# Kernel optimization log

Measured on AMD Instinct MI355X. Metric: run time of the kernel, lower is better.

## Reference

```python
import jax, jax.numpy as jnp
import numpy as np

B, N, D_IN, D_OUT = 4, 2048, 4096, 4096
E, R, D_ATT = 8, 16, 128
SCALING = 16.0 / 16.0  # alpha / rank


def setup_inputs() -> dict:
    key = jax.random.key(0)
    ks = jax.random.split(key, 8)
    x = jax.random.normal(ks[0], (B, N, D_IN), dtype=jnp.float32)
    weight = jax.random.normal(ks[1], (D_OUT, D_IN), dtype=jnp.float32) * 0.02  # frozen base
    bias = jax.random.normal(ks[2], (D_OUT,), dtype=jnp.float32) * 0.02
    router_V = jax.random.normal(ks[3], (D_ATT, D_IN), dtype=jnp.float32) * 0.02
    router_U = jax.random.normal(ks[4], (D_ATT, D_IN), dtype=jnp.float32) * 0.02
    router_W = jax.random.normal(ks[5], (E, D_ATT), dtype=jnp.float32) * 0.02
    experts_A = jax.random.normal(ks[6], (E, D_IN, R), dtype=jnp.float32) * 0.01
    experts_B = jax.random.normal(ks[7], (E, R, D_OUT), dtype=jnp.float32) * 0.01
    return {"x": x, "weight": weight, "bias": bias, "router_V": router_V,
            "router_U": router_U, "router_W": router_W,
            "experts_A": experts_A, "experts_B": experts_B}


def reference(x, weight, bias, router_V, router_U, router_W, experts_A, experts_B):
    # Frozen base projection: F.linear(x, weight, bias)
    base = jnp.einsum('bnd,od->bno', x, weight) + bias
    # ABMIL gated-attention router
    v = jnp.tanh(jnp.einsum('bnd,ad->bna', x, router_V))            # [B,N,D_att]
    u = jax.nn.sigmoid(jnp.einsum('bnd,ad->bna', x, router_U))      # [B,N,D_att]
    scores = jnp.einsum('bna,ea->bne', v * u, router_W)             # [B,N,E]
    router_weights = jax.nn.sigmoid(scores)                         # independent sigmoid gates
    # Per-expert low-rank path (dropout is identity at inference / p=0)
    lora_down = jnp.einsum('bnd,edr->bner', x, experts_A)           # [B,N,E,R]
    weighted = lora_down * router_weights[..., None]
    moe_out = jnp.einsum('bner,erd->bnd', weighted, experts_B)      # [B,N,D_out]
    return base + SCALING * moe_out
```

## Files before the change

### kernel.cpp

```cpp
#include <hip/hip_runtime.h>
#include <hip/hip_bf16.h>

#define M_TOT   8192
#define D_IN    4096
#define D_OUT   4096
#define N_E     8
#define N_R     16
#define D_ATT   128
#define ER      128
#define CATN    384
#define KEXT    4224

typedef __attribute__((ext_vector_type(8))) __bf16 bf16x8;
typedef __attribute__((ext_vector_type(4))) float  f32x4;

__device__ __forceinline__ ushort f2bf(float f) {
  union { float f; unsigned u; } v; v.f = f;
  unsigned r = (v.u + 0x7fffu + ((v.u >> 16) & 1u)) >> 16;
  return (ushort)r;
}

__global__ void f2bf4_kernel(const float* __restrict__ in, ushort* __restrict__ out, long n4) {
  long i = blockIdx.x * (long)blockDim.x + threadIdx.x;
  if (i >= n4) return;
  const float4 a = reinterpret_cast<const float4*>(in)[i];
  ushort4 r; r.x = f2bf(a.x); r.y = f2bf(a.y); r.z = f2bf(a.z); r.w = f2bf(a.w);
  reinterpret_cast<ushort4*>(out)[i] = r;
}

__global__ void f2bf4s_kernel(const float* __restrict__ in, ushort* __restrict__ out, long n4) {
  long i = blockIdx.x * (long)blockDim.x + threadIdx.x;
  if (i >= n4) return;
  const float4 a = reinterpret_cast<const float4*>(in)[i];
  ushort4 r; r.x = f2bf(a.x); r.y = f2bf(a.y); r.z = f2bf(a.z); r.w = f2bf(a.w);
  long row = i >> 10, c4 = (i & 1023) << 2;
  *reinterpret_cast<ushort4*>(out + row * KEXT + c4) = r;
}

__global__ void prep_catA_kernel(const float* __restrict__ expA, ushort* __restrict__ cat) {
  int idx = blockIdx.x * 256 + threadIdx.x;
  int j = idx >> 12, d = idx & 4095;
  int e = j >> 4, r = j & 15;
  cat[(size_t)(2 * D_ATT + j) * D_IN + d] = f2bf(expA[((size_t)e * D_IN + d) * N_R + r]);
}

__global__ void prep_bt_kernel(const float* __restrict__ expB, ushort* __restrict__ we) {
  int idx = blockIdx.x * 256 + threadIdx.x;
  int j = idx >> 12, o = idx & 4095;
  we[(size_t)o * KEXT + D_IN + j] = f2bf(expB[(size_t)j * D_OUT + o]);
}

__global__ void gate_kernel(const float* __restrict__ P, const float* __restrict__ rW,
                            ushort* __restrict__ wtd) {
  int token = blockIdx.x * 4 + (threadIdx.x >> 6);
  int l = threadIdx.x & 63;
  const float* p = P + (size_t)token * CATN;
  float v0 = tanhf(p[l]);
  float v1 = tanhf(p[l + 64]);
  float u0 = 1.f / (1.f + __expf(-p[D_ATT + l]));
  float u1 = 1.f / (1.f + __expf(-p[D_ATT + l + 64]));
  float g0 = v0 * u0, g1 = v1 * u1;
  float rw[8];
  #pragma unroll
  for (int e = 0; e < 8; ++e) {
    float s = g0 * rW[e * D_ATT + l] + g1 * rW[e * D_ATT + l + 64];
    #pragma unroll
    for (int off = 32; off > 0; off >>= 1) s += __shfl_xor(s, off);
    rw[e] = 1.f / (1.f + __expf(-s));
  }
  int q = l >> 4;
  float rw_a = (q == 0) ? rw[0] : (q == 1) ? rw[1] : (q == 2) ? rw[2] : rw[3];
  float rw_b = (q == 0) ? rw[4] : (q == 1) ? rw[5] : (q == 2) ? rw[6] : rw[7];
  wtd[(size_t)token * KEXT + l]      = f2bf(p[2 * D_ATT + l]      * rw_a);
  wtd[(size_t)token * KEXT + l + 64] = f2bf(p[2 * D_ATT + l + 64] * rw_b);
}

__global__ __launch_bounds__(256, 2)
void gemm128_kernel(const ushort* __restrict__ A, const ushort* __restrict__ Bm,
                    float* __restrict__ C, int Ncols, int K, int lda, int ldb)
{
  __shared__ ushort As[128 * 64];
  __shared__ ushort Bs[128 * 64];
  const int tid = threadIdx.x;
  const int w = tid >> 6, l = tid & 63;
  const int wr = w >> 1, wc = w & 1;
  const int l16 = l & 15, lq = l >> 4;
  const int brow = blockIdx.y * 128;
  const int bcol = blockIdx.x * 128;

  f32x4 acc[4][4] = {};
  const int nk = K >> 6;

  for (int kt = 0; kt < nk; ++kt) {
    int k0 = kt << 6;
    #pragma unroll
    for (int c = 0; c < 4; ++c) {
      int rloc = w * 32 + c * 8;
      int rl = rloc + (l >> 3);
      int kk = k0 + (l & 7) * 8;
      const ushort* ga = A  + (size_t)(brow + rl) * lda + kk;
      const ushort* gb = Bm + (size_t)(bcol + rl) * ldb + kk;
      __builtin_amdgcn_global_load_lds((const __attribute__((address_space(1))) void*)ga,
                                       (__attribute__((address_space(3))) void*)(As + rloc * 64),
                                       16, 0, 0);
      __builtin_amdgcn_global_load_lds((const __attribute__((address_space(1))) void*)gb,
                                       (__attribute__((address_space(3))) void*)(Bs + rloc * 64),
                                       16, 0, 0);
    }
    __syncthreads();

    #pragma unroll
    for (int ks = 0; ks < 2; ++ks) {
      bf16x8 af[4], bfv[4];
      #pragma unroll
      for (int mi = 0; mi < 4; ++mi)
        af[mi] = *reinterpret_cast<const bf16x8*>(As + (wr * 64 + mi * 16 + l16) * 64 + ks * 32 + lq * 8);
      #pragma unroll
      for (int ni = 0; ni < 4; ++ni)
        bfv[ni] = *reinterpret_cast<const bf16x8*>(Bs + (wc * 64 + ni * 16 + l16) * 64 + ks * 32 + lq * 8);
      #pragma unroll
      for (int mi = 0; mi < 4; ++mi)
        #pragma unroll
        for (int ni = 0; ni < 4; ++ni)
          acc[mi][ni] = __builtin_amdgcn_mfma_f32_16x16x32_bf16(af[mi], bfv[ni], acc[mi][ni], 0, 0, 0);
    }
    __syncthreads();
  }

  #pragma unroll
  for (int ni = 0; ni < 4; ++ni) {
    int col = bcol + wc * 64 + ni * 16 + l16;
    #pragma unroll
    for (int mi = 0; mi < 4; ++mi) {
      f32x4 v = acc[mi][ni];
      int row0 = brow + wr * 64 + mi * 16 + lq * 4;
      #pragma unroll
      for (int j = 0; j < 4; ++j)
        C[(size_t)(row0 + j) * Ncols + col] = v[j];
    }
  }
}

__global__ __launch_bounds__(512, 2)
void gemm256_kernel(const ushort* __restrict__ A, const ushort* __restrict__ Bm,
                    float* __restrict__ C, const float* __restrict__ bias,
                    int Ncols, int K, int ld, int ntm)
{
  __shared__ ushort lds[2][2][2][8192];
  const int tid = threadIdx.x;
  const int wid = tid >> 6, l = tid & 63;
  const int wr = wid >> 2, wc = wid & 3;
  const int l16 = l & 15, lq = l >> 4;
  const int rxor = (l16 & 7) << 3;

  const int cpx = gridDim.x >> 3;
  const int sid = ((int)blockIdx.x & 7) * cpx + ((int)blockIdx.x >> 3);
  const int brow = (sid % ntm) * 256;
  const int bcol = (sid / ntm) * 256;

  const int NT = K >> 6;

  const int srow = tid >> 3;
  const int scol = (((tid & 7) ^ ((tid >> 3) & 7)) << 3);

#define STAGE(buf_, mat_, half_, kt_) do {                                        \
    const ushort* _s = (mat_) ? Bm : A;                                           \
    int _rb = ((mat_) ? bcol : brow) + (half_) * 128 + srow;                      \
    ushort* _d = &lds[(buf_)][(mat_)][(half_)][wid * 512];                        \
    _Pragma("unroll")                                                             \
    for (int _c = 0; _c < 2; ++_c) {                                              \
      const ushort* _g = _s + (size_t)(_rb + _c * 64) * ld + (kt_) * 64 + scol;   \
      __builtin_amdgcn_global_load_lds(                                           \
          (const __attribute__((address_space(1))) void*)_g,                      \
          (__attribute__((address_space(3))) void*)(_d + _c * 4096), 16, 0, 0);   \
    } } while (0)

#define LDA_FRAG(buf_, mi_, ks_) \
  (*reinterpret_cast<const bf16x8*>(&lds[(buf_)][0][wr][((mi_) * 16 + l16) * 64 + (((ks_) * 32 + lq * 8) ^ rxor)]))
#define LDB_FRAG(buf_, ni_, ks_) \
  (*reinterpret_cast<const bf16x8*>(&lds[(buf_)][1][wc >> 1][((wc & 1) * 64 + (ni_) * 16 + l16) * 64 + (((ks_) * 32 + lq * 8) ^ rxor)]))

  f32x4 acc[8][4] = {};

  STAGE(0, 0, 0, 0); STAGE(0, 0, 1, 0);
  STAGE(0, 1, 0, 0); STAGE(0, 1, 1, 0);
  {
    const int k1 = (NT > 1) ? 1 : 0;
    STAGE(1, 1, 0, k1); STAGE(1, 1, 1, k1);
  }
  asm volatile("s_waitcnt vmcnt(4)" ::: "memory");
  __builtin_amdgcn_s_barrier();

  for (int t = 0; t < NT; ++t) {
    const int buf = t & 1;
    const int ktA = (t + 1 < NT) ? t + 1 : NT - 1;
    const int ktB = (t + 2 < NT) ? t + 2 : NT - 1;
    bf16x8 af[4][2], b0[2][2], b1[2][2];

    #pragma unroll
    for (int mi = 0; mi < 4; ++mi)
      #pragma unroll
      for (int ks = 0; ks < 2; ++ks)
        af[mi][ks] = LDA_FRAG(buf, mi, ks);
    #pragma unroll
    for (int ni = 0; ni < 2; ++ni)
      #pragma unroll
      for (int ks = 0; ks < 2; ++ks)
        b0[ni][ks] = LDB_FRAG(buf, ni, ks);
    STAGE(buf ^ 1, 0, 0, ktA);
    __builtin_amdgcn_s_barrier();
    asm volatile("s_waitcnt lgkmcnt(0)" ::: "memory");
    __builtin_amdgcn_s_setprio(1);
    #pragma unroll
    for (int mi = 0; mi < 4; ++mi)
      #pragma unroll
      for (int ni = 0; ni < 2; ++ni)
        #pragma unroll
        for (int ks = 0; ks < 2; ++ks)
          acc[mi][ni] = __builtin_amdgcn_mfma_f32_16x16x32_bf16(af[mi][ks], b0[ni][ks], acc[mi][ni], 0, 0, 0);
    __builtin_amdgcn_s_setprio(0);
    __builtin_amdgcn_s_barrier();

    #pragma unroll
    for (int ni = 0; ni < 2; ++ni)
      #pragma unroll
      for (int ks = 0; ks < 2; ++ks)
        b1[ni][ks] = LDB_FRAG(buf, ni + 2, ks);
    STAGE(buf ^ 1, 0, 1, ktA);
    __builtin_amdgcn_s_barrier();
    asm volatile("s_waitcnt lgkmcnt(0)" ::: "memory");
    __builtin_amdgcn_s_setprio(1);
    #pragma unroll
    for (int mi = 0; mi < 4; ++mi)
      #pragma unroll
      for (int ni = 0; ni < 2; ++ni)
        #pragma unroll
        for (int ks = 0; ks < 2; ++ks)
          acc[mi][ni + 2] = __builtin_amdgcn_mfma_f32_16x16x32_bf16(af[mi][ks], b1[ni][ks], acc[mi][ni + 2], 0, 0, 0);
    __builtin_amdgcn_s_setprio(0);
    __builtin_amdgcn_s_barrier();

    #pragma unroll
    for (int mi = 0; mi < 4; ++mi)
      #pragma unroll
      for (int ks = 0; ks < 2; ++ks)
        af[mi][ks] = LDA_FRAG(buf, mi + 4, ks);
    STAGE(buf, 1, 0, ktB);
    __builtin_amdgcn_s_barrier();
    asm volatile("s_waitcnt lgkmcnt(0)" ::: "memory");
    __builtin_amdgcn_s_setprio(1);
    #pragma unroll
    for (int mi = 0; mi < 4; ++mi)
      #pragma unroll
      for (int ni = 0; ni < 2; ++ni)
        #pragma unroll
        for (int ks = 0; ks < 2; ++ks)
          acc[mi + 4][ni + 2] = __builtin_amdgcn_mfma_f32_16x16x32_bf16(af[mi][ks], b1[ni][ks], acc[mi + 4][ni + 2], 0, 0, 0);
    __builtin_amdgcn_s_setprio(0);
    __builtin_amdgcn_s_barrier();

    STAGE(buf, 1, 1, ktB);
    asm volatile("s_waitcnt vmcnt(4)" ::: "memory");
    __builtin_amdgcn_s_barrier();
    __builtin_amdgcn_s_setprio(1);
    #pragma unroll
    for (int mi = 0; mi < 4; ++mi)
      #pragma unroll
      for (int ni = 0; ni < 2; ++ni)
        #pragma unroll
        for (int ks = 0; ks < 2; ++ks)
          acc[mi + 4][ni] = __builtin_amdgcn_mfma_f32_16x16x32_bf16(af[mi][ks], b0[ni][ks], acc[mi + 4][ni], 0, 0, 0);
    __builtin_amdgcn_s_setprio(0);
    __builtin_amdgcn_s_barrier();
  }

  asm volatile("s_waitcnt vmcnt(0)" ::: "memory");

  #pragma unroll
  for (int ni = 0; ni < 4; ++ni) {
    int col = bcol + wc * 64 + ni * 16 + l16;
    float bs = bias[col];
    #pragma unroll
    for (int mi = 0; mi < 8; ++mi) {
      int row0 = brow + wr * 128 + mi * 16 + lq * 4;
      #pragma unroll
      for (int j = 0; j < 4; ++j)
        C[(size_t)(row0 + j) * Ncols + col] = acc[mi][ni][j] + bs;
    }
  }
#undef STAGE
#undef LDA_FRAG
#undef LDB_FRAG
}

extern "C" void kernel_launch(void* const* d_in, const int* in_sizes, int n_in,
                              void* d_out, int out_size, void* d_ws, size_t ws_size,
                              hipStream_t stream) {
  const float* x      = (const float*)d_in[0];
  const float* weight = (const float*)d_in[1];
  const float* bias   = (const float*)d_in[2];
  const float* rV     = (const float*)d_in[3];
  const float* rU     = (const float*)d_in[4];
  const float* rW     = (const float*)d_in[5];
  const float* expA   = (const float*)d_in[6];
  const float* expB   = (const float*)d_in[7];
  float* out = (float*)d_out;

  ushort* xe  = (ushort*)d_ws;
  ushort* we  = xe  + (size_t)M_TOT * KEXT;
  ushort* cat = we  + (size_t)D_OUT * KEXT;
  float*  P   = (float*)(cat + (size_t)CATN * D_IN);

  long n4;
  n4 = (long)M_TOT * D_IN / 4;
  f2bf4s_kernel<<<dim3((n4 + 255) / 256), 256, 0, stream>>>(x, xe, n4);
  n4 = (long)D_OUT * D_IN / 4;
  f2bf4s_kernel<<<dim3((n4 + 255) / 256), 256, 0, stream>>>(weight, we, n4);
  n4 = (long)D_ATT * D_IN / 4;
  f2bf4_kernel<<<dim3((n4 + 255) / 256), 256, 0, stream>>>(rV, cat, n4);
  f2bf4_kernel<<<dim3((n4 + 255) / 256), 256, 0, stream>>>(rU, cat + (size_t)D_ATT * D_IN, n4);
  prep_catA_kernel<<<dim3(ER * D_IN / 256), 256, 0, stream>>>(expA, cat);
  prep_bt_kernel<<<dim3(ER * D_OUT / 256), 256, 0, stream>>>(expB, we);

  gemm128_kernel<<<dim3(CATN / 128, M_TOT / 128), 256, 0, stream>>>(
      xe, cat, P, CATN, D_IN, KEXT, D_IN);

  gate_kernel<<<dim3(M_TOT / 4), 256, 0, stream>>>(P, rW, xe + D_IN);

  gemm256_kernel<<<dim3((D_OUT / 256) * (M_TOT / 256)), 512, 0, stream>>>(
      xe, we, out, bias, D_OUT, KEXT, KEXT, M_TOT / 256);
}
```

Measured before the change: 405.1 us.

## Software-pipeline LDS fragment reads across tiles and hardcode GEMM dimensions

Restructures the main 256x256 GEMM loop so the next tile's low A/B fragments are read from LDS during the current tile's last MFMA phase, with ping-pong register sets and a loop unrolled by two. The high-B and high-A fragments are now loaded inside the MFMA phases instead of before the barriers. All shapes and strides become compile-time constants in both GEMMs, which lets the compiler simplify address arithmetic. The intent is to hide LDS read latency behind MFMA work, at the cost of more live fragment registers at two waves per SIMD and a loop that assumes an even tile count.

```diff
diff --git a/kernel.cpp b/kernel.cpp
--- a/kernel.cpp
+++ b/kernel.cpp
@@ -10,6 +10,8 @@
 #define ER      128
 #define CATN    384
 #define KEXT    4224
+#define NTK     66
+#define NTM     32
 
 typedef __attribute__((ext_vector_type(8))) __bf16 bf16x8;
 typedef __attribute__((ext_vector_type(4))) float  f32x4;
@@ -77,7 +79,7 @@
 
 __global__ __launch_bounds__(256, 2)
 void gemm128_kernel(const ushort* __restrict__ A, const ushort* __restrict__ Bm,
-                    float* __restrict__ C, int Ncols, int K, int lda, int ldb)
+                    float* __restrict__ C)
 {
   __shared__ ushort As[128 * 64];
   __shared__ ushort Bs[128 * 64];
@@ -89,17 +91,16 @@
   const int bcol = blockIdx.x * 128;
 
   f32x4 acc[4][4] = {};
-  const int nk = K >> 6;
-
-  for (int kt = 0; kt < nk; ++kt) {
+
+  for (int kt = 0; kt < (D_IN >> 6); ++kt) {
     int k0 = kt << 6;
     #pragma unroll
     for (int c = 0; c < 4; ++c) {
       int rloc = w * 32 + c * 8;
       int rl = rloc + (l >> 3);
       int kk = k0 + (l & 7) * 8;
-      const ushort* ga = A  + (size_t)(brow + rl) * lda + kk;
-      const ushort* gb = Bm + (size_t)(bcol + rl) * ldb + kk;
+      const ushort* ga = A  + (size_t)(brow + rl) * KEXT + kk;
+      const ushort* gb = Bm + (size_t)(bcol + rl) * D_IN + kk;
       __builtin_amdgcn_global_load_lds((const __attribute__((address_space(1))) void*)ga,
                                        (__attribute__((address_space(3))) void*)(As + rloc * 64),
                                        16, 0, 0);
@@ -136,15 +137,14 @@
       int row0 = brow + wr * 64 + mi * 16 + lq * 4;
       #pragma unroll
       for (int j = 0; j < 4; ++j)
-        C[(size_t)(row0 + j) * Ncols + col] = v[j];
+        C[(size_t)(row0 + j) * CATN + col] = v[j];
     }
   }
 }
 
 __global__ __launch_bounds__(512, 2)
 void gemm256_kernel(const ushort* __restrict__ A, const ushort* __restrict__ Bm,
-                    float* __restrict__ C, const float* __restrict__ bias,
-                    int Ncols, int K, int ld, int ntm)
+                    float* __restrict__ C, const float* __restrict__ bias)
 {
   __shared__ ushort lds[2][2][2][8192];
   const int tid = threadIdx.x;
@@ -153,12 +153,10 @@
   const int l16 = l & 15, lq = l >> 4;
   const int rxor = (l16 & 7) << 3;
 
-  const int cpx = gridDim.x >> 3;
+  const int cpx = (NTM * (D_OUT / 256)) >> 3;
   const int sid = ((int)blockIdx.x & 7) * cpx + ((int)blockIdx.x >> 3);
-  const int brow = (sid % ntm) * 256;
-  const int bcol = (sid / ntm) * 256;
-
-  const int NT = K >> 6;
+  const int brow = (sid % NTM) * 256;
+  const int bcol = (sid / NTM) * 256;
 
   const int srow = tid >> 3;
   const int scol = (((tid & 7) ^ ((tid >> 3) & 7)) << 3);
@@ -169,7 +167,7 @@
     ushort* _d = &lds[(buf_)][(mat_)][(half_)][wid * 512];                        \
     _Pragma("unroll")                                                             \
     for (int _c = 0; _c < 2; ++_c) {                                              \
-      const ushort* _g = _s + (size_t)(_rb + _c * 64) * ld + (kt_) * 64 + scol;   \
+      const ushort* _g = _s + (size_t)(_rb + _c * 64) * KEXT + (kt_) * 64 + scol; \
       __builtin_amdgcn_global_load_lds(                                           \
           (const __attribute__((address_space(1))) void*)_g,                      \
           (__attribute__((address_space(3))) void*)(_d + _c * 4096), 16, 0, 0);   \
@@ -180,101 +178,84 @@
 #define LDB_FRAG(buf_, ni_, ks_) \
   (*reinterpret_cast<const bf16x8*>(&lds[(buf_)][1][wc >> 1][((wc & 1) * 64 + (ni_) * 16 + l16) * 64 + (((ks_) * 32 + lq * 8) ^ rxor)]))
 
+#define RD_ALO(buf_, dst_) \
+    _Pragma("unroll") for (int mi = 0; mi < 4; ++mi) \
+      _Pragma("unroll") for (int ks = 0; ks < 2; ++ks) dst_[mi][ks] = LDA_FRAG(buf_, mi, ks);
+#define RD_BLO(buf_, dst_) \
+    _Pragma("unroll") for (int ni = 0; ni < 2; ++ni) \
+      _Pragma("unroll") for (int ks = 0; ks < 2; ++ks) dst_[ni][ks] = LDB_FRAG(buf_, ni, ks);
+
+#define MFMA_Q(accm0_, accn0_, a_, b_) \
+    _Pragma("unroll") for (int mi = 0; mi < 4; ++mi) \
+      _Pragma("unroll") for (int ni = 0; ni < 2; ++ni) \
+        _Pragma("unroll") for (int ks = 0; ks < 2; ++ks) \
+          acc[(accm0_) + mi][(accn0_) + ni] = __builtin_amdgcn_mfma_f32_16x16x32_bf16( \
+              a_[mi][ks], b_[ni][ks], acc[(accm0_) + mi][(accn0_) + ni], 0, 0, 0);
+
+#define TILE(t_, buf_, aIn_, b0In_, aOut_, b0Out_) do {                           \
+    bf16x8 b1[2][2], aHi[4][2];                                                   \
+    const int ktA = ((t_) + 1 < NTK) ? (t_) + 1 : NTK - 1;                        \
+    const int ktB = ((t_) + 2 < NTK) ? (t_) + 2 : NTK - 1;                        \
+                                                                          \
+    STAGE(buf_ ^ 1, 0, 0, ktA);                                                   \
+    __builtin_amdgcn_s_barrier();                                                 \
+    asm volatile("s_waitcnt lgkmcnt(0)" ::: "memory");                            \
+    __builtin_amdgcn_s_setprio(1);                                                \
+    _Pragma("unroll") for (int ni = 0; ni < 2; ++ni)                              \
+      _Pragma("unroll") for (int ks = 0; ks < 2; ++ks)                            \
+        b1[ni][ks] = LDB_FRAG(buf_, ni + 2, ks);                                  \
+    MFMA_Q(0, 0, aIn_, b0In_);                                                    \
+    __builtin_amdgcn_s_setprio(0);                                                \
+    __builtin_amdgcn_s_barrier();                                                 \
+                                                                          \
+    STAGE(buf_ ^ 1, 0, 1, ktA);                                                   \
+    __builtin_amdgcn_s_barrier();                                                 \
+    asm volatile("s_waitcnt lgkmcnt(0)" ::: "memory");                            \
+    __builtin_amdgcn_s_setprio(1);                                                \
+    _Pragma("unroll") for (int mi = 0; mi < 4; ++mi)                              \
+      _Pragma("unroll") for (int ks = 0; ks < 2; ++ks)                            \
+        aHi[mi][ks] = LDA_FRAG(buf_, mi + 4, ks);                                 \
+    MFMA_Q(0, 2, aIn_, b1);                                                       \
+    __builtin_amdgcn_s_setprio(0);                                                \
+    __builtin_amdgcn_s_barrier();                                                 \
+                                                                          \
+    STAGE(buf_, 1, 0, ktB);                                                       \
+    __builtin_amdgcn_s_barrier();                                                 \
+    asm volatile("s_waitcnt lgkmcnt(0)" ::: "memory");                            \
+    __builtin_amdgcn_s_setprio(1);                                                \
+    MFMA_Q(4, 2, aHi, b1);                                                        \
+    __builtin_amdgcn_s_setprio(0);                                                \
+    __builtin_amdgcn_s_barrier();                                                 \
+                                                                          \
+    STAGE(buf_, 1, 1, ktB);                                                       \
+    asm volatile("s_waitcnt vmcnt(4)" ::: "memory");                              \
+    __builtin_amdgcn_s_barrier();                                                 \
+    __builtin_amdgcn_s_setprio(1);                                                \
+    RD_ALO(buf_ ^ 1, aOut_);                                                      \
+    RD_BLO(buf_ ^ 1, b0Out_);                                                     \
+    MFMA_Q(4, 0, aHi, b0In_);                                                     \
+    __builtin_amdgcn_s_setprio(0);                                                \
+    __builtin_amdgcn_s_barrier();                                                 \
+  } while (0)
+
   f32x4 acc[8][4] = {};
+  bf16x8 aA[4][2], b0A[2][2], aB[4][2], b0B[2][2];
 
   STAGE(0, 0, 0, 0); STAGE(0, 0, 1, 0);
   STAGE(0, 1, 0, 0); STAGE(0, 1, 1, 0);
-  {
-    const int k1 = (NT > 1) ? 1 : 0;
-    STAGE(1, 1, 0, k1); STAGE(1, 1, 1, k1);
-  }
+  STAGE(1, 1, 0, 1); STAGE(1, 1, 1, 1);
   asm volatile("s_waitcnt vmcnt(4)" ::: "memory");
   __builtin_amdgcn_s_barrier();
-
-  for (int t = 0; t < NT; ++t) {
-    const int buf = t & 1;
-    const int ktA = (t + 1 < NT) ? t + 1 : NT - 1;
-    const int ktB = (t + 2 < NT) ? t + 2 : NT - 1;
-    bf16x8 af[4][2], b0[2][2], b1[2][2];
-
-    #pragma unroll
-    for (int mi = 0; mi < 4; ++mi)
-      #pragma unroll
-      for (int ks = 0; ks < 2; ++ks)
-        af[mi][ks] = LDA_FRAG(buf, mi, ks);
-    #pragma unroll
-    for (int ni = 0; ni < 2; ++ni)
-      #pragma unroll
-      for (int ks = 0; ks < 2; ++ks)
-        b0[ni][ks] = LDB_FRAG(buf, ni, ks);
-    STAGE(buf ^ 1, 0, 0, ktA);
-    __builtin_amdgcn_s_barrier();
-    asm volatile("s_waitcnt lgkmcnt(0)" ::: "memory");
-    __builtin_amdgcn_s_setprio(1);
-    #pragma unroll
-    for (int mi = 0; mi < 4; ++mi)
-      #pragma unroll
-      for (int ni = 0; ni < 2; ++ni)
-        #pragma unroll
-        for (int ks = 0; ks < 2; ++ks)
-          acc[mi][ni] = __builtin_amdgcn_mfma_f32_16x16x32_bf16(af[mi][ks], b0[ni][ks], acc[mi][ni], 0, 0, 0);
-    __builtin_amdgcn_s_setprio(0);
-    __builtin_amdgcn_s_barrier();
-
-    #pragma unroll
-    for (int ni = 0; ni < 2; ++ni)
-      #pragma unroll
-      for (int ks = 0; ks < 2; ++ks)
-        b1[ni][ks] = LDB_FRAG(buf, ni + 2, ks);
-    STAGE(buf ^ 1, 0, 1, ktA);
-    __builtin_amdgcn_s_barrier();
-    asm volatile("s_waitcnt lgkmcnt(0)" ::: "memory");
-    __builtin_amdgcn_s_setprio(1);
-    #pragma unroll
-    for (int mi = 0; mi < 4; ++mi)
-      #pragma unroll
-      for (int ni = 0; ni < 2; ++ni)
-        #pragma unroll
-        for (int ks = 0; ks < 2; ++ks)
-          acc[mi][ni + 2] = __builtin_amdgcn_mfma_f32_16x16x32_bf16(af[mi][ks], b1[ni][ks], acc[mi][ni + 2], 0, 0, 0);
-    __builtin_amdgcn_s_setprio(0);
-    __builtin_amdgcn_s_barrier();
-
-    #pragma unroll
-    for (int mi = 0; mi < 4; ++mi)
-      #pragma unroll
-      for (int ks = 0; ks < 2; ++ks)
-        af[mi][ks] = LDA_FRAG(buf, mi + 4, ks);
-    STAGE(buf, 1, 0, ktB);
-    __builtin_amdgcn_s_barrier();
-    asm volatile("s_waitcnt lgkmcnt(0)" ::: "memory");
-    __builtin_amdgcn_s_setprio(1);
-    #pragma unroll
-    for (int mi = 0; mi < 4; ++mi)
-      #pragma unroll
-      for (int ni = 0; ni < 2; ++ni)
-        #pragma unroll
-        for (int ks = 0; ks < 2; ++ks)
-          acc[mi + 4][ni + 2] = __builtin_amdgcn_mfma_f32_16x16x32_bf16(af[mi][ks], b1[ni][ks], acc[mi + 4][ni + 2], 0, 0, 0);
-    __builtin_amdgcn_s_setprio(0);
-    __builtin_amdgcn_s_barrier();
-
-    STAGE(buf, 1, 1, ktB);
-    asm volatile("s_waitcnt vmcnt(4)" ::: "memory");
-    __builtin_amdgcn_s_barrier();
-    __builtin_amdgcn_s_setprio(1);
-    #pragma unroll
-    for (int mi = 0; mi < 4; ++mi)
-      #pragma unroll
-      for (int ni = 0; ni < 2; ++ni)
-        #pragma unroll
-        for (int ks = 0; ks < 2; ++ks)
-          acc[mi + 4][ni] = __builtin_amdgcn_mfma_f32_16x16x32_bf16(af[mi][ks], b0[ni][ks], acc[mi + 4][ni], 0, 0, 0);
-    __builtin_amdgcn_s_setprio(0);
-    __builtin_amdgcn_s_barrier();
-  }
-
-  asm volatile("s_waitcnt vmcnt(0)" ::: "memory");
+  RD_ALO(0, aA);
+  RD_BLO(0, b0A);
+
+  #pragma unroll 1
+  for (int tp = 0; tp < NTK / 2; ++tp) {
+    TILE(2 * tp,     0, aA, b0A, aB, b0B);
+    TILE(2 * tp + 1, 1, aB, b0B, aA, b0A);
+  }
+
+  asm volatile("s_waitcnt vmcnt(0) lgkmcnt(0)" ::: "memory");
 
   #pragma unroll
   for (int ni = 0; ni < 4; ++ni) {
@@ -285,12 +266,16 @@
       int row0 = brow + wr * 128 + mi * 16 + lq * 4;
       #pragma unroll
       for (int j = 0; j < 4; ++j)
-        C[(size_t)(row0 + j) * Ncols + col] = acc[mi][ni][j] + bs;
+        C[(size_t)(row0 + j) * D_OUT + col] = acc[mi][ni][j] + bs;
     }
   }
 #undef STAGE
 #undef LDA_FRAG
 #undef LDB_FRAG
+#undef RD_ALO
+#undef RD_BLO
+#undef MFMA_Q
+#undef TILE
 }
 
 extern "C" void kernel_launch(void* const* d_in, const int* in_sizes, int n_in,
@@ -322,11 +307,9 @@
   prep_catA_kernel<<<dim3(ER * D_IN / 256), 256, 0, stream>>>(expA, cat);
   prep_bt_kernel<<<dim3(ER * D_OUT / 256), 256, 0, stream>>>(expB, we);
 
-  gemm128_kernel<<<dim3(CATN / 128, M_TOT / 128), 256, 0, stream>>>(
-      xe, cat, P, CATN, D_IN, KEXT, D_IN);
+  gemm128_kernel<<<dim3(CATN / 128, M_TOT / 128), 256, 0, stream>>>(xe, cat, P);
 
   gate_kernel<<<dim3(M_TOT / 4), 256, 0, stream>>>(P, rW, xe + D_IN);
 
-  gemm256_kernel<<<dim3((D_OUT / 256) * (M_TOT / 256)), 512, 0, stream>>>(
-      xe, we, out, bias, D_OUT, KEXT, KEXT, M_TOT / 256);
-}
+  gemm256_kernel<<<dim3((D_OUT / 256) * (M_TOT / 256)), 512, 0, stream>>>(xe, we, out, bias);
+}
```

After: 401.4 us. No clear change (-0.9%).
